# Kernel optimization log

Hardware: AMD Instinct MI355X
Metric: run time of the kernel (lower is better)

## Reference

```python
import jax, jax.numpy as jnp
import numpy as np

EPS = 1e-8

def _apply_norms(x):
    # x: [B, C, H, W]; torch .std() is unbiased (ddof=1)
    x_min = x.min(axis=1, keepdims=True)
    x_max = x.max(axis=1, keepdims=True)
    norm_minmax = (x - x_min) / (x_max - x_min + EPS)
    x_mean = x.mean(axis=1, keepdims=True)
    x_std = x.std(axis=1, keepdims=True, ddof=1)
    norm_z = (x - x_mean) / (x_std + EPS)
    b_mean = x.mean(axis=(0, 2, 3), keepdims=True)
    b_std = x.std(axis=(0, 2, 3), keepdims=True, ddof=1)
    norm_bn = (x - b_mean) / (b_std + EPS)
    return [norm_minmax, norm_z, norm_bn]

def _compute_metrics(pred, targ):
    B, C, H, W = pred.shape
    p = pred.reshape(B, C, H * W)
    t = targ.reshape(B, C, H * W)
    # SAM: 1 - cosine similarity over channel dim (torch clamps norms at eps)
    dot = (p * t).sum(axis=1)
    np_ = jnp.maximum(jnp.sqrt((p * p).sum(axis=1)), EPS)
    nt_ = jnp.maximum(jnp.sqrt((t * t).sum(axis=1)), EPS)
    sam = 1.0 - dot / (np_ * nt_)
    # Pearson over channel dim
    p_ctr = p - p.mean(axis=1, keepdims=True)
    t_ctr = t - t.mean(axis=1, keepdims=True)
    cov = (p_ctr * t_ctr).sum(axis=1)
    std_p = jnp.sqrt((p_ctr ** 2).sum(axis=1) + EPS)
    std_t = jnp.sqrt((t_ctr ** 2).sum(axis=1) + EPS)
    pearson = 1.0 - cov / (std_p * std_t)
    # SID: symmetric KL over channel-normalized positive distributions
    p_pos = p - p.min(axis=1, keepdims=True)
    t_pos = t - t.min(axis=1, keepdims=True)
    p_prob = jnp.maximum(p_pos / (p_pos.sum(axis=1, keepdims=True) + EPS), EPS)
    t_prob = jnp.maximum(t_pos / (t_pos.sum(axis=1, keepdims=True) + EPS), EPS)
    log_ratio = jnp.log(p_prob / t_prob)
    d_pt = (p_prob * log_ratio).sum(axis=1)
    d_tp = (t_prob * (-log_ratio)).sum(axis=1)
    sid = d_pt + d_tp
    return sam, pearson, sid  # each [B, H*W]

TOP_K_RATIO = 0.05

def setup_inputs() -> dict:
    key = jax.random.key(0)
    k1, k2 = jax.random.split(key)
    B, C, H, W = 4, 128, 256, 256
    reconstructed = jax.random.normal(k1, (B, C, H, W), dtype=jnp.float32)
    target = jax.random.normal(k2, (B, C, H, W), dtype=jnp.float32)
    loss_weights = jnp.ones((9,), dtype=jnp.float32)
    return {"reconstructed": reconstructed, "target": target, "loss_weights": loss_weights}

def reference(reconstructed, target, loss_weights):
    B, C, H, W = reconstructed.shape
    preds = _apply_norms(reconstructed)
    targs = _apply_norms(target)
    all_losses = []
    for p_norm, t_norm in zip(preds, targs):
        sam, pearson, sid = _compute_metrics(p_norm, t_norm)
        all_losses.extend([sam, pearson, sid])
    stacked = jnp.stack(all_losses, axis=0)  # [9, B, H*W]
    weights = jax.nn.softmax(loss_weights).reshape(9, 1, 1)
    weighted_error_map = (stacked * weights).sum(axis=0)  # [B, H*W]
    err_flat = weighted_error_map.reshape(-1)
    k = max(1, int(err_flat.shape[0] * TOP_K_RATIO))
    top_k_errors, _ = jax.lax.top_k(err_flat, k)
    return jnp.mean(top_k_errors), weighted_error_map.reshape(B, H, W)
```

## Files before the change

### kernel.cpp

```cpp
#include <hip/hip_runtime.h>

#define EPSF 1e-8f
#define CCH 128
#define HWSZ 65536
#define NPIX 262144
#define KTOP 13107
#define LN2F 0.6931471805599453f

#define WS_CST    512
#define WS_WGT    1024
#define WS_MINKEY 1040
#define WS_MAXKEY 1041
#define WS_BSTAR  1042
#define WS_CNTAB  1043
#define WS_LO2    1044
#define WS_W2     1045
#define WS_K2     1046
#define WS_SUMAB  1048
#define WS_H1     1056
#define WS_H2C    5152
#define WS_H2S    9248
#define WS_TOTAL  13344

__device__ __forceinline__ unsigned fkey(float f){
  unsigned u = __float_as_uint(f);
  return (u & 0x80000000u) ? ~u : (u | 0x80000000u);
}
__device__ __forceinline__ float funkey(unsigned k){
  unsigned u = (k & 0x80000000u) ? (k & 0x7fffffffu) : ~k;
  return __uint_as_float(u);
}

struct Stats {
  float psum,psumsq,tsum,tsumsq,ptsum,pmin,pmax,tmin,tmax;
  float bS1,bS11,bS2,bS22,bS12,bMp,bMt;
};
struct Consts { float errBase,fp,Bp,ft,Bt,fbp,Bbp,fbt,Bbt,sidW,bnW; };

__device__ Consts pixEpilogue(const Stats& s, const float* wgt){
  const float Ci = 1.0f/128.0f;
  float smm_p = 1.f/(s.pmax-s.pmin+EPSF);
  float smm_t = 1.f/(s.tmax-s.tmin+EPSF);
  float mean_p = s.psum*Ci, mean_t = s.tsum*Ci;
  float var_p = fmaxf((s.psumsq - s.psum*s.psum*Ci)*(1.f/127.f), 0.f);
  float var_t = fmaxf((s.tsumsq - s.tsum*s.tsum*Ci)*(1.f/127.f), 0.f);
  float zi_p = 1.f/(sqrtf(var_p)+EPSF);
  float zi_t = 1.f/(sqrtf(var_t)+EPSF);

  auto metrics = [&](float S1,float S11,float S2,float S22,float S12,
                     float& sam,float& pear){
    float npn = fmaxf(sqrtf(fmaxf(S11,0.f)), EPSF);
    float ntn = fmaxf(sqrtf(fmaxf(S22,0.f)), EPSF);
    sam = 1.f - S12/(npn*ntn);
    float cov = S12 - S1*S2*Ci;
    float vp = fmaxf(S11 - S1*S1*Ci, 0.f);
    float vt = fmaxf(S22 - S2*S2*Ci, 0.f);
    pear = 1.f - cov/(sqrtf(vp+EPSF)*sqrtf(vt+EPSF));
  };
  auto affine = [&](float ap,float sp,float at,float st,float& sam,float& pear){
    float S1 = (s.psum - 128.f*ap)*sp;
    float S11 = (s.psumsq - 2.f*ap*s.psum + 128.f*ap*ap)*sp*sp;
    float S2 = (s.tsum - 128.f*at)*st;
    float S22 = (s.tsumsq - 2.f*at*s.tsum + 128.f*at*at)*st*st;
    float S12 = (s.ptsum - at*s.psum - ap*s.tsum + 128.f*ap*at)*sp*st;
    metrics(S1,S11,S2,S22,S12,sam,pear);
  };

  float sam_mm,pear_mm,sam_z,pear_z,sam_bn,pear_bn;
  affine(s.pmin,smm_p,s.tmin,smm_t,sam_mm,pear_mm);
  affine(mean_p,zi_p,mean_t,zi_t,sam_z,pear_z);
  metrics(s.bS1,s.bS11,s.bS2,s.bS22,s.bS12,sam_bn,pear_bn);

  Consts c;
  c.errBase = wgt[0]*sam_mm + wgt[1]*pear_mm + wgt[3]*sam_z + wgt[4]*pear_z
            + wgt[6]*sam_bn + wgt[7]*pear_bn;
  float dp = fmaf(s.psum - 128.f*s.pmin, smm_p, EPSF);
  c.fp = smm_p/dp;  c.Bp = s.pmin*c.fp;
  float dt = fmaf(s.tsum - 128.f*s.tmin, smm_t, EPSF);
  c.ft = smm_t/dt;  c.Bt = s.tmin*c.ft;
  c.fbp = 1.f/((s.bS1 - 128.f*s.bMp) + EPSF); c.Bbp = s.bMp*c.fbp;
  c.fbt = 1.f/((s.bS2 - 128.f*s.bMt) + EPSF); c.Bbt = s.bMt*c.fbt;
  c.sidW = (wgt[2]+wgt[5])*LN2F;
  c.bnW  = wgt[8]*LN2F;
  return c;
}

__global__ __launch_bounds__(256) void initWs(unsigned* __restrict__ wsu){
  int idx = blockIdx.x*256 + threadIdx.x;
  if (idx < WS_TOTAL) wsu[idx] = (idx == WS_MINKEY) ? 0xFFFFFFFFu : 0u;
}

__global__ __launch_bounds__(256, 4) void chSumKernel(const float* __restrict__ rec,
                                                      const float* __restrict__ tgt,
                                                      float* __restrict__ wsf){
  __shared__ float acc[16][512];
  int tid = threadIdx.x;
  int pix0 = blockIdx.x*512 + tid*2;
  int b = pix0 >> 16;
  unsigned hwb = (unsigned)(pix0 & (HWSZ-1)) * 4u;
  const char* pB = (const char*)(rec + ((size_t)b*CCH)*HWSZ) + hwb;
  const char* tB = (const char*)(tgt + ((size_t)b*CCH)*HWSZ) + hwb;
  int lane = tid & 63, w = tid >> 6;
  int grp = w*4 + (lane>>4);

  for (int cb=0; cb<CCH; cb+=8){
    float2 P[8], T[8];
    #pragma unroll
    for (int j=0;j<8;j++){
      P[j] = *(const float2*)(pB + ((unsigned)(cb+j)<<18));
      T[j] = *(const float2*)(tB + ((unsigned)(cb+j)<<18));
    }
    #pragma unroll
    for (int j=0;j<8;j++){
      asm volatile("" : "+v"(P[j].x), "+v"(P[j].y), "+v"(T[j].x), "+v"(T[j].y));
    }
    #pragma unroll
    for (int j=0;j<8;j++){
      float sp = P[j].x + P[j].y;
      float qp = fmaf(P[j].x,P[j].x, P[j].y*P[j].y);
      float st = T[j].x + T[j].y;
      float qt = fmaf(T[j].x,T[j].x, T[j].y*T[j].y);
      #pragma unroll
      for (int off=1; off<16; off<<=1){
        sp += __shfl_xor(sp,off); qp += __shfl_xor(qp,off);
        st += __shfl_xor(st,off); qt += __shfl_xor(qt,off);
      }
      if ((lane&15)==0){
        int c4 = (cb+j)*4;
        acc[grp][c4+0]=sp; acc[grp][c4+1]=qp; acc[grp][c4+2]=st; acc[grp][c4+3]=qt;
      }
    }
  }
  __syncthreads();
  int sh = (blockIdx.x & 7)*512;
  for (int i=tid; i<512; i+=256){
    float v = 0.f;
    #pragma unroll
    for (int g=0; g<16; g++) v += acc[g][i];
    atomicAdd(&wsf[WS_H1 + sh + i], v);
  }
}

__global__ __launch_bounds__(256) void finalizeKernel(const float* __restrict__ lw,
                                                      float* __restrict__ wsf){
  int tid = threadIdx.x;
  if (tid < 128){
    int c = tid;
    float sp=0,qp=0,st=0,qt=0;
    #pragma unroll
    for (int s=0;s<8;s++){
      const float* shp = wsf + WS_H1 + s*512 + c*4;
      sp += shp[0]; qp += shp[1]; st += shp[2]; qt += shp[3];
    }
    const float N = 262144.f;
    float mean_p = sp/N;
    float var_p = fmaxf((qp - sp*sp/N)/(N-1.f), 0.f);
    float inv_p = 1.f/(sqrtf(var_p)+EPSF);
    float mean_t = st/N;
    float var_t = fmaxf((qt - st*st/N)/(N-1.f), 0.f);
    float inv_t = 1.f/(sqrtf(var_t)+EPSF);
    wsf[WS_CST + c*4 + 0] = inv_p;
    wsf[WS_CST + c*4 + 1] = mean_p*inv_p;
    wsf[WS_CST + c*4 + 2] = inv_t;
    wsf[WS_CST + c*4 + 3] = mean_t*inv_t;
  }
  if (tid==0){
    float m = -1e30f;
    for (int i=0;i<9;i++) m = fmaxf(m, lw[i]);
    float e[9], sum=0.f;
    for (int i=0;i<9;i++){ e[i]=expf(lw[i]-m); sum+=e[i]; }
    for (int i=0;i<9;i++) wsf[WS_WGT+i] = e[i]/sum;
  }
  __syncthreads();
  for (int i=tid; i<4096; i+=256) wsf[WS_H1+i] = 0.f;
}

__global__ __launch_bounds__(256, 4) void mainKernel(const float* __restrict__ rec,
                                                     const float* __restrict__ tgt,
                                                     const float* __restrict__ wsf,
                                                     unsigned* __restrict__ wsu,
                                                     float* __restrict__ errMap){
  __shared__ float4 cst[128];
  __shared__ float wgtS[12];
  __shared__ float rmn[4], rmx[4];
  int tid = threadIdx.x;
  if (tid < 128) cst[tid] = ((const float4*)(wsf + WS_CST))[tid];
  if (tid < 9)  wgtS[tid] = wsf[WS_WGT + tid];
  __syncthreads();

  int pix0 = blockIdx.x*512 + tid*2;
  int b = pix0 >> 16;
  unsigned hwb = (unsigned)(pix0 & (HWSZ-1)) * 4u;
  const char* pB = (const char*)(rec + ((size_t)b*CCH)*HWSZ) + hwb;
  const char* tB = (const char*)(tgt + ((size_t)b*CCH)*HWSZ) + hwb;

  float2 psum={0,0},psumsq={0,0},tsum={0,0},tsumsq={0,0},ptsum={0,0};
  float2 pmin={3.4e38f,3.4e38f},pmax={-3.4e38f,-3.4e38f};
  float2 tmin={3.4e38f,3.4e38f},tmax={-3.4e38f,-3.4e38f};
  float2 bS1={0,0},bS11={0,0},bS2={0,0},bS22={0,0},bS12={0,0};
  float2 bMp={3.4e38f,3.4e38f},bMt={3.4e38f,3.4e38f};

  for (int cb=0; cb<CCH; cb+=8){
    float2 P[8], T[8];
    #pragma unroll
    for (int j=0;j<8;j++){
      P[j] = *(const float2*)(pB + ((unsigned)(cb+j)<<18));
      T[j] = *(const float2*)(tB + ((unsigned)(cb+j)<<18));
    }
    #pragma unroll
    for (int j=0;j<8;j++){
      asm volatile("" : "+v"(P[j].x), "+v"(P[j].y), "+v"(T[j].x), "+v"(T[j].y));
    }
    #pragma unroll
    for (int j=0;j<8;j++){
      float4 k = cst[cb+j];
      float2 pv=P[j], tv=T[j];
      psum.x+=pv.x; psum.y+=pv.y;
      psumsq.x=fmaf(pv.x,pv.x,psumsq.x); psumsq.y=fmaf(pv.y,pv.y,psumsq.y);
      tsum.x+=tv.x; tsum.y+=tv.y;
      tsumsq.x=fmaf(tv.x,tv.x,tsumsq.x); tsumsq.y=fmaf(tv.y,tv.y,tsumsq.y);
      ptsum.x=fmaf(pv.x,tv.x,ptsum.x); ptsum.y=fmaf(pv.y,tv.y,ptsum.y);
      pmin.x=fminf(pmin.x,pv.x); pmin.y=fminf(pmin.y,pv.y);
      pmax.x=fmaxf(pmax.x,pv.x); pmax.y=fmaxf(pmax.y,pv.y);
      tmin.x=fminf(tmin.x,tv.x); tmin.y=fminf(tmin.y,tv.y);
      tmax.x=fmaxf(tmax.x,tv.x); tmax.y=fmaxf(tmax.y,tv.y);
      float bpx = fmaf(pv.x,k.x,-k.y), bpy = fmaf(pv.y,k.x,-k.y);
      float btx = fmaf(tv.x,k.z,-k.w), bty = fmaf(tv.y,k.z,-k.w);
      bS1.x+=bpx; bS1.y+=bpy;
      bS11.x=fmaf(bpx,bpx,bS11.x); bS11.y=fmaf(bpy,bpy,bS11.y);
      bS2.x+=btx; bS2.y+=bty;
      bS22.x=fmaf(btx,btx,bS22.x); bS22.y=fmaf(bty,bty,bS22.y);
      bS12.x=fmaf(bpx,btx,bS12.x); bS12.y=fmaf(bpy,bty,bS12.y);
      bMp.x=fminf(bMp.x,bpx); bMp.y=fminf(bMp.y,bpy);
      bMt.x=fminf(bMt.x,btx); bMt.y=fminf(bMt.y,bty);
    }
  }

  Stats sx = {psum.x,psumsq.x,tsum.x,tsumsq.x,ptsum.x,pmin.x,pmax.x,tmin.x,tmax.x,
              bS1.x,bS11.x,bS2.x,bS22.x,bS12.x,bMp.x,bMt.x};
  Stats sy = {psum.y,psumsq.y,tsum.y,tsumsq.y,ptsum.y,pmin.y,pmax.y,tmin.y,tmax.y,
              bS1.y,bS11.y,bS2.y,bS22.y,bS12.y,bMp.y,bMt.y};
  Consts cx = pixEpilogue(sx, wgtS);
  Consts cy = pixEpilogue(sy, wgtS);

  float2 sid_mm={0,0}, sid_bn={0,0};
  for (int cb=0; cb<CCH; cb+=8){
    float2 P[8], T[8];
    #pragma unroll
    for (int j=0;j<8;j++){
      P[j] = *(const float2*)(pB + ((unsigned)(cb+j)<<18));
      T[j] = *(const float2*)(tB + ((unsigned)(cb+j)<<18));
    }
    #pragma unroll
    for (int j=0;j<8;j++){
      asm volatile("" : "+v"(P[j].x), "+v"(P[j].y), "+v"(T[j].x), "+v"(T[j].y));
    }
    #pragma unroll
    for (int j=0;j<8;j++){
      float4 k = cst[cb+j];
      float2 pv=P[j], tv=T[j];
      float ppx = fmaxf(fmaf(pv.x,cx.fp,-cx.Bp), EPSF);
      float tpx = fmaxf(fmaf(tv.x,cx.ft,-cx.Bt), EPSF);
      sid_mm.x = fmaf(ppx-tpx, __log2f(ppx)-__log2f(tpx), sid_mm.x);
      float ppy = fmaxf(fmaf(pv.y,cy.fp,-cy.Bp), EPSF);
      float tpy = fmaxf(fmaf(tv.y,cy.ft,-cy.Bt), EPSF);
      sid_mm.y = fmaf(ppy-tpy, __log2f(ppy)-__log2f(tpy), sid_mm.y);
      float bpx = fmaf(pv.x,k.x,-k.y), bpy = fmaf(pv.y,k.x,-k.y);
      float btx = fmaf(tv.x,k.z,-k.w), bty = fmaf(tv.y,k.z,-k.w);
      float qpx = fmaxf(fmaf(bpx,cx.fbp,-cx.Bbp), EPSF);
      float qtx = fmaxf(fmaf(btx,cx.fbt,-cx.Bbt), EPSF);
      sid_bn.x = fmaf(qpx-qtx, __log2f(qpx)-__log2f(qtx), sid_bn.x);
      float qpy = fmaf(bpy,cy.fbp,-cy.Bbp);  qpy = fmaxf(qpy, EPSF);
      float qty = fmaf(bty,cy.fbt,-cy.Bbt);  qty = fmaxf(qty, EPSF);
      sid_bn.y = fmaf(qpy-qty, __log2f(qpy)-__log2f(qty), sid_bn.y);
    }
  }

  float errx = cx.errBase + cx.sidW*sid_mm.x + cx.bnW*sid_bn.x;
  float erry = cy.errBase + cy.sidW*sid_mm.y + cy.bnW*sid_bn.y;
  errMap[pix0]   = errx;
  errMap[pix0+1] = erry;

  float emin = fminf(errx,erry), emax = fmaxf(errx,erry);
  #pragma unroll
  for (int off=1; off<64; off<<=1){
    emin = fminf(emin, __shfl_xor(emin,off));
    emax = fmaxf(emax, __shfl_xor(emax,off));
  }
  int w = tid>>6;
  if ((tid&63)==0){ rmn[w]=emin; rmx[w]=emax; }
  __syncthreads();
  if (tid==0){
    emin = fminf(fminf(rmn[0],rmn[1]),fminf(rmn[2],rmn[3]));
    emax = fmaxf(fmaxf(rmx[0],rmx[1]),fmaxf(rmx[2],rmx[3]));
    atomicMin(&wsu[WS_MINKEY], fkey(emin));
    atomicMax(&wsu[WS_MAXKEY], fkey(emax));
  }
}

__global__ __launch_bounds__(256) void hist1Kernel(const float* __restrict__ err,
                                                   unsigned* __restrict__ wsu){
  __shared__ unsigned h[4096];
  int tid = threadIdx.x;
  for (int i=tid;i<4096;i+=256) h[i]=0u;
  __syncthreads();
  float lo = funkey(wsu[WS_MINKEY]);
  float hi = funkey(wsu[WS_MAXKEY]);
  float invw = 4096.f / fmaxf(hi-lo, 1e-30f);
  int base = blockIdx.x*2048 + tid;
  for (int j=0;j<8;j++){
    float v = err[base + j*256];
    int idx = (int)fminf(fmaxf((v-lo)*invw, 0.f), 4095.f);
    atomicAdd(&h[idx], 1u);
  }
  __syncthreads();
  for (int i=tid;i<4096;i+=256){ unsigned c=h[i]; if (c) atomicAdd(&wsu[WS_H1+i], c); }
}

__global__ __launch_bounds__(256) void scan1Kernel(float* __restrict__ wsf,
                                                   unsigned* __restrict__ wsu){
  __shared__ unsigned counts[4096];
  __shared__ unsigned s[256];
  int tid = threadIdx.x;
  for (int i=tid;i<4096;i+=256) counts[i]=wsu[WS_H1+i];
  __syncthreads();
  unsigned part=0;
  for (int j=0;j<16;j++) part += counts[tid*16+j];
  s[tid]=part; __syncthreads();
  for (int off=1; off<256; off<<=1){
    unsigned v = (tid+off<256)? s[tid+off] : 0u;
    __syncthreads();
    s[tid] += v;
    __syncthreads();
  }
  float lo = funkey(wsu[WS_MINKEY]);
  float hi = funkey(wsu[WS_MAXKEY]);
  float w1 = fmaxf(hi-lo, 1e-30f) * (1.f/4096.f);
  unsigned cum = (tid<255)? s[tid+1] : 0u;
  for (int j=15;j>=0;j--){
    int bin = tid*16+j;
    unsigned cn = cum + counts[bin];
    if (cum < (unsigned)KTOP && cn >= (unsigned)KTOP){
      wsu[WS_BSTAR] = (unsigned)bin;
      wsu[WS_CNTAB] = cum;
      wsu[WS_K2]    = (unsigned)KTOP - cum;
      wsf[WS_LO2]   = lo + (float)bin*w1;
      wsf[WS_W2]    = w1*(1.f/4096.f);
    }
    cum = cn;
  }
}

__global__ __launch_bounds__(256) void hist2Kernel(const float* __restrict__ err,
                                                   float* __restrict__ wsf,
                                                   unsigned* __restrict__ wsu){
  __shared__ unsigned h2[4096];
  __shared__ float s2[4096];
  __shared__ float ls[4];
  int tid = threadIdx.x;
  for (int i=tid;i<4096;i+=256){ h2[i]=0u; s2[i]=0.f; }
  __syncthreads();
  float lo = funkey(wsu[WS_MINKEY]);
  float hi = funkey(wsu[WS_MAXKEY]);
  float invw = 4096.f / fmaxf(hi-lo, 1e-30f);
  int bstar = (int)wsu[WS_BSTAR];
  float lo2 = wsf[WS_LO2];
  float w2  = wsf[WS_W2];
  float invw2 = 1.f / w2;
  float mySum = 0.f;
  int base = blockIdx.x*2048 + tid;
  for (int j=0;j<8;j++){
    float v = err[base + j*256];
    int idx = (int)fminf(fmaxf((v-lo)*invw, 0.f), 4095.f);
    if (idx > bstar){
      mySum += v;
    } else if (idx == bstar){
      int i2 = (int)fminf(fmaxf((v-lo2)*invw2, 0.f), 4095.f);
      atomicAdd(&h2[i2], 1u);
      atomicAdd(&s2[i2], v);
    }
  }
  for (int off=1; off<64; off<<=1) mySum += __shfl_xor(mySum, off);
  if ((tid&63)==0) ls[tid>>6] = mySum;
  __syncthreads();
  if (tid==0) atomicAdd(&wsf[WS_SUMAB], ls[0]+ls[1]+ls[2]+ls[3]);
  for (int i=tid;i<4096;i+=256){
    unsigned c = h2[i]; if (c) atomicAdd(&wsu[WS_H2C+i], c);
    float sv = s2[i];   if (sv != 0.f) atomicAdd(&wsf[WS_H2S+i], sv);
  }
}

__global__ __launch_bounds__(256) void scan2Kernel(float* __restrict__ wsf,
                                                   unsigned* __restrict__ wsu,
                                                   float* __restrict__ out){
  __shared__ unsigned cnt[4096];
  __shared__ float sm[4096];
  __shared__ unsigned sC[256];
  __shared__ float sS[256];
  int tid = threadIdx.x;
  for (int i=tid;i<4096;i+=256){ cnt[i]=wsu[WS_H2C+i]; sm[i]=wsf[WS_H2S+i]; }
  __syncthreads();
  unsigned pc=0; float ps=0.f;
  for (int j=0;j<16;j++){ pc+=cnt[tid*16+j]; ps+=sm[tid*16+j]; }
  sC[tid]=pc; sS[tid]=ps; __syncthreads();
  for (int off=1; off<256; off<<=1){
    unsigned vc = (tid+off<256)? sC[tid+off] : 0u;
    float vs    = (tid+off<256)? sS[tid+off] : 0.f;
    __syncthreads();
    sC[tid] += vc; sS[tid] += vs;
    __syncthreads();
  }
  unsigned k2 = wsu[WS_K2];
  float lo2 = wsf[WS_LO2], w2 = wsf[WS_W2];
  unsigned cum = (tid<255)? sC[tid+1] : 0u;
  float cums   = (tid<255)? sS[tid+1] : 0.f;
  for (int j=15;j>=0;j--){
    int bin = tid*16+j;
    unsigned cn = cum + cnt[bin];
    float sn = cums + sm[bin];
    if (cum < k2 && cn >= k2){
      float val = lo2 + ((float)bin + 0.5f)*w2;
      float total = wsf[WS_SUMAB] + cums + (float)(k2 - cum)*val;
      out[0] = total / (float)KTOP;
    }
    cum = cn; cums = sn;
  }
}

extern "C" void kernel_launch(void* const* d_in, const int* in_sizes, int n_in,
                              void* d_out, int out_size, void* d_ws, size_t ws_size,
                              hipStream_t stream){
  const float* rec = (const float*)d_in[0];
  const float* tgt = (const float*)d_in[1];
  const float* lw  = (const float*)d_in[2];
  float* out = (float*)d_out;
  float* wsf = (float*)d_ws;
  unsigned* wsu = (unsigned*)d_ws;

  hipLaunchKernelGGL(initWs, dim3((WS_TOTAL+255)/256), dim3(256), 0, stream, wsu);
  hipLaunchKernelGGL(chSumKernel, dim3(NPIX/512), dim3(256), 0, stream, rec, tgt, wsf);
  hipLaunchKernelGGL(finalizeKernel, dim3(1), dim3(256), 0, stream, lw, wsf);
  hipLaunchKernelGGL(mainKernel, dim3(NPIX/512), dim3(256), 0, stream, rec, tgt, wsf, wsu, out+1);
  hipLaunchKernelGGL(hist1Kernel, dim3(128), dim3(256), 0, stream, out+1, wsu);
  hipLaunchKernelGGL(scan1Kernel, dim3(1), dim3(256), 0, stream, wsf, wsu);
  hipLaunchKernelGGL(hist2Kernel, dim3(128), dim3(256), 0, stream, out+1, wsf, wsu);
  hipLaunchKernelGGL(scan2Kernel, dim3(1), dim3(256), 0, stream, wsf, wsu, out);
}
```

Before: 194.1 us.

## Replace pixel-tiled channel-stats kernel with contiguous chunk streaming reduction

The per-channel batch statistics pass now walks each tensor in contiguous 16 KB chunks, where each chunk belongs to one (batch, channel) plane. Each block reduces its chunk's sum and sum of squares with float4 loads, then issues two atomics into sharded per-channel slots. The previous kernel read strided float2 loads across all channels per pixel tile and used a large shared accumulator. The new layout targets fully coalesced wide loads at the cost of more block-level syncs and atomics per chunk.

Measured after the change: 167.3 us. 1.16x faster.

```diff
diff --git a/kernel.cpp b/kernel.cpp
--- a/kernel.cpp
+++ b/kernel.cpp
@@ -90,54 +90,39 @@
   if (idx < WS_TOTAL) wsu[idx] = (idx == WS_MINKEY) ? 0xFFFFFFFFu : 0u;
 }
 
-__global__ __launch_bounds__(256, 4) void chSumKernel(const float* __restrict__ rec,
-                                                      const float* __restrict__ tgt,
-                                                      float* __restrict__ wsf){
-  __shared__ float acc[16][512];
-  int tid = threadIdx.x;
-  int pix0 = blockIdx.x*512 + tid*2;
-  int b = pix0 >> 16;
-  unsigned hwb = (unsigned)(pix0 & (HWSZ-1)) * 4u;
-  const char* pB = (const char*)(rec + ((size_t)b*CCH)*HWSZ) + hwb;
-  const char* tB = (const char*)(tgt + ((size_t)b*CCH)*HWSZ) + hwb;
-  int lane = tid & 63, w = tid >> 6;
-  int grp = w*4 + (lane>>4);
-
-  for (int cb=0; cb<CCH; cb+=8){
-    float2 P[8], T[8];
-    #pragma unroll
-    for (int j=0;j<8;j++){
-      P[j] = *(const float2*)(pB + ((unsigned)(cb+j)<<18));
-      T[j] = *(const float2*)(tB + ((unsigned)(cb+j)<<18));
-    }
-    #pragma unroll
-    for (int j=0;j<8;j++){
-      asm volatile("" : "+v"(P[j].x), "+v"(P[j].y), "+v"(T[j].x), "+v"(T[j].y));
-    }
-    #pragma unroll
-    for (int j=0;j<8;j++){
-      float sp = P[j].x + P[j].y;
-      float qp = fmaf(P[j].x,P[j].x, P[j].y*P[j].y);
-      float st = T[j].x + T[j].y;
-      float qt = fmaf(T[j].x,T[j].x, T[j].y*T[j].y);
-      #pragma unroll
-      for (int off=1; off<16; off<<=1){
-        sp += __shfl_xor(sp,off); qp += __shfl_xor(qp,off);
-        st += __shfl_xor(st,off); qt += __shfl_xor(qt,off);
-      }
-      if ((lane&15)==0){
-        int c4 = (cb+j)*4;
-        acc[grp][c4+0]=sp; acc[grp][c4+1]=qp; acc[grp][c4+2]=st; acc[grp][c4+3]=qt;
-      }
-    }
-  }
-  __syncthreads();
-  int sh = (blockIdx.x & 7)*512;
-  for (int i=tid; i<512; i+=256){
-    float v = 0.f;
-    #pragma unroll
-    for (int g=0; g<16; g++) v += acc[g][i];
-    atomicAdd(&wsf[WS_H1 + sh + i], v);
+__global__ __launch_bounds__(256) void streamStatsKernel(const float* __restrict__ rec,
+                                                         const float* __restrict__ tgt,
+                                                         float* __restrict__ wsf){
+  __shared__ float ws_[4], wq_[4];
+  int tid = threadIdx.x;
+  for (int ch = blockIdx.x; ch < 16384; ch += 2048){
+    int tensor = ch >> 13;
+    int ci = ch & 8191;
+    const float4* base = (const float4*)(tensor ? tgt : rec) + (size_t)ci*1024;
+    float4 L0 = base[tid];
+    float4 L1 = base[tid + 256];
+    float4 L2 = base[tid + 512];
+    float4 L3 = base[tid + 768];
+    float s = ((L0.x+L0.y)+(L0.z+L0.w)) + ((L1.x+L1.y)+(L1.z+L1.w))
+            + ((L2.x+L2.y)+(L2.z+L2.w)) + ((L3.x+L3.y)+(L3.z+L3.w));
+    float q = (fmaf(L0.x,L0.x,L0.y*L0.y) + fmaf(L0.z,L0.z,L0.w*L0.w))
+            + (fmaf(L1.x,L1.x,L1.y*L1.y) + fmaf(L1.z,L1.z,L1.w*L1.w))
+            + (fmaf(L2.x,L2.x,L2.y*L2.y) + fmaf(L2.z,L2.z,L2.w*L2.w))
+            + (fmaf(L3.x,L3.x,L3.y*L3.y) + fmaf(L3.z,L3.z,L3.w*L3.w));
+    #pragma unroll
+    for (int off=1; off<64; off<<=1){ s += __shfl_xor(s,off); q += __shfl_xor(q,off); }
+    int w = tid>>6;
+    if ((tid&63)==0){ ws_[w]=s; wq_[w]=q; }
+    __syncthreads();
+    if (tid==0){
+      float S = ws_[0]+ws_[1]+ws_[2]+ws_[3];
+      float Q = wq_[0]+wq_[1]+wq_[2]+wq_[3];
+      int c = (ci >> 4) & 127;
+      int sh = blockIdx.x & 7;
+      atomicAdd(&wsf[WS_H1 + sh*512 + tensor*256 + c], S);
+      atomicAdd(&wsf[WS_H1 + sh*512 + tensor*256 + 128 + c], Q);
+    }
+    __syncthreads();
   }
 }
 
@@ -149,8 +134,9 @@
     float sp=0,qp=0,st=0,qt=0;
     #pragma unroll
     for (int s=0;s<8;s++){
-      const float* shp = wsf + WS_H1 + s*512 + c*4;
-      sp += shp[0]; qp += shp[1]; st += shp[2]; qt += shp[3];
+      const float* shp = wsf + WS_H1 + s*512;
+      sp += shp[c];       qp += shp[128+c];
+      st += shp[256+c];   qt += shp[384+c];
     }
     const float N = 262144.f;
     float mean_p = sp/N;
@@ -438,7 +424,7 @@
   unsigned* wsu = (unsigned*)d_ws;
 
   hipLaunchKernelGGL(initWs, dim3((WS_TOTAL+255)/256), dim3(256), 0, stream, wsu);
-  hipLaunchKernelGGL(chSumKernel, dim3(NPIX/512), dim3(256), 0, stream, rec, tgt, wsf);
+  hipLaunchKernelGGL(streamStatsKernel, dim3(2048), dim3(256), 0, stream, rec, tgt, wsf);
   hipLaunchKernelGGL(finalizeKernel, dim3(1), dim3(256), 0, stream, lw, wsf);
   hipLaunchKernelGGL(mainKernel, dim3(NPIX/512), dim3(256), 0, stream, rec, tgt, wsf, wsu, out+1);
   hipLaunchKernelGGL(hist1Kernel, dim3(128), dim3(256), 0, stream, out+1, wsu);
```
